# Optimization experiments

Hardware: AMD Instinct MI355X
Metric: run time of the kernel (lower is better)

The kernel has to match this reference:

```python
import jax, jax.numpy as jnp
from jax import lax
import numpy as np
from functools import partial

B, C, H, W = 4, 3, 256, 256
HW = H * W
KCAP = 32          # max tracked components per (batch, class) slot
MAX_ITER = 5
KSIZE = 5


def _depthwise_sum(x, k):
    c = x.shape[1]
    w = jnp.ones((c, 1, k, k), x.dtype)
    return lax.conv_general_dilated(x, w, (1, 1), [(k // 2, k // 2)] * 2,
                                    feature_group_count=c,
                                    dimension_numbers=('NCHW', 'OIHW', 'NCHW'))


def erode(x):
    return (_depthwise_sum(x, KSIZE) >= KSIZE * KSIZE - 0.5).astype(x.dtype)


def dilate(x):
    return (_depthwise_sum(x, KSIZE) > 0.5).astype(x.dtype)


def _maxpool3_int(L):
    return lax.reduce_window(L, jnp.int32(0), lax.max, (1, 1, 3, 3), (1, 1, 1, 1),
                             [(0, 0), (0, 0), (1, 1), (1, 1)])


def label_cc(binary):
    # connected-component labeling by iterated 3x3 max-pool of pixel indices,
    # exactly as find_components_max_pool (labels = max flat pixel index in comp)
    b = lax.stop_gradient(binary) > 0.5
    idx = jnp.arange(HW, dtype=jnp.int32).reshape(1, 1, H, W)
    L0 = jnp.where(b, idx, 0)

    def cond(st):
        return st[1]

    def body(st):
        L, _ = st
        Ln = jnp.where(b, _maxpool3_int(L), 0)
        return Ln, jnp.any(Ln != L)

    L, _ = lax.while_loop(cond, body, (L0, jnp.array(True)))
    return L


def extract_components(Lf, binf):
    # per (b,c): top-KCAP components sorted by comp.sum() = size*label/maxL (desc)
    flat = Lf.reshape(-1)
    sizes = jnp.zeros((HW,), jnp.float32).at[flat].add(binf.reshape(-1))
    idx = jnp.arange(HW, dtype=jnp.int32)
    is_root = (flat == idx) & (flat > 0)  # label 0 excluded, as in torch code
    key = jnp.where(is_root, lax.stop_gradient(sizes) * idx.astype(jnp.float32), -1.0)
    _, top_lab = lax.top_k(key, KCAP)
    valid = key[top_lab] > 0.0
    maxL = jnp.maximum(flat.max(), 1).astype(jnp.float32)
    v = top_lab.astype(jnp.float32)
    s = jnp.where(valid, sizes[top_lab] * v / maxL, 0.0)  # comp.sum()
    lab = jnp.where(valid, top_lab, -1)
    # component tensor = mask * label/maxL, exactly mask*L/max(L) of the original
    comps = (Lf[None] == lab[:, None, None]).astype(jnp.float32) * (v / maxL)[:, None, None]
    return s, comps, valid


def process_step(P, n, bar, s, comps, valid, t):
    # overlaps vs components stored BEFORE this step; new comps within a step
    # are pixel-disjoint so they can never match each other (overlap == 0).
    OV = jnp.einsum('jhw,khw->jk', comps, P)

    def body(carry, inp):
        P, n, bar = carry
        s_j, comp_j, valid_j, ov_j = inp
        best = jnp.argmax(ov_j)
        matched = ov_j[best] > 0.0
        widx = jnp.clip(jnp.where(matched, best, n), 0, KCAP - 1)
        can = valid_j & (matched | (n < KCAP))
        bar = bar.at[widx, t].set(jnp.where(can, s_j, bar[widx, t]))
        add = valid_j & (~matched) & (n < KCAP)
        nw = jnp.minimum(n, KCAP - 1)
        P = P.at[nw].set(jnp.where(add, comp_j, P[nw]))
        return (P, n + add.astype(n.dtype), bar), None

    (P, n, bar), _ = lax.scan(body, (P, n, bar), (s, comps, valid, OV))
    return P, n, bar


def compute_barcodes(binary):
    half = MAX_ITER // 2
    seq = [(binary, half)]
    m = binary
    for t in range(half):
        m = erode(m)
        seq.append((m, half + t + 1))
    m = binary
    for t in range(half):
        m = dilate(m)
        seq.append((m, half - t - 1))
    BC = B * C
    P = jnp.zeros((BC, KCAP, H, W), jnp.float32)
    n = jnp.zeros((BC,), jnp.int32)
    bar = jnp.zeros((BC, KCAP, MAX_ITER), jnp.float32)
    for mp, t in seq:  # fixed 5-step schedule (structural loop)
        L = label_cc(mp).reshape(BC, H, W)
        s, comps, valid = jax.vmap(extract_components)(L, mp.reshape(BC, H, W))
        P, n, bar = jax.vmap(partial(process_step, t=t))(P, n, bar, s, comps, valid)
    return bar.reshape(B, C, KCAP, MAX_ITER), n.reshape(B, C)


def topo_forward(predictions, gumbel, targets):
    y_soft = jax.nn.softmax(predictions + gumbel, axis=1)
    hard = jax.nn.one_hot(jnp.argmax(y_soft, axis=1), C, axis=1, dtype=jnp.float32)
    binary_pred = hard + y_soft - lax.stop_gradient(y_soft)  # straight-through
    binary_tgt = jnp.moveaxis(jax.nn.one_hot(targets, C, dtype=jnp.float32), -1, 1)
    bp, n_p = compute_barcodes(binary_pred)
    bt, n_t = compute_barcodes(binary_tgt)
    k = jnp.arange(KCAP)
    valid_p = k[None, None] < n_p[:, :, None]
    has_t = k[None, None] < n_t[:, :, None]
    pmax = bp.max(-1)
    pmax = jnp.where(pmax > 0, pmax, 1.0)
    tgt = jnp.where(has_t[..., None], bt, 0.0)
    term = jnp.sum((tgt - bp) ** 2, -1) / pmax ** 2
    losses = jnp.sum(jnp.where(valid_p, term, 0.0), axis=(1, 2))
    return losses.mean()  # reduction='mean'


def setup_inputs() -> dict:
    key = jax.random.key(0)
    k1, k2, k3 = jax.random.split(key, 3)
    # blob-like logits: low-res noise upsampled so component counts stay < KCAP
    lo = jax.random.normal(k1, (B, C, 16, 16), jnp.float32)
    predictions = 8.0 * jax.image.resize(lo, (B, C, H, W), 'linear')
    lo_t = jax.random.normal(k2, (B, C, 16, 16), jnp.float32)
    targets = jnp.argmax(jax.image.resize(lo_t, (B, C, H, W), 'linear'), axis=1).astype(jnp.int32)
    u = jax.random.uniform(k3, (B, C, H, W), jnp.float32, minval=1e-6, maxval=1.0 - 1e-6)
    gumbel = -jnp.log(-jnp.log(u))  # standard Gumbel noise (F.gumbel_softmax)
    return {"predictions": predictions, "gumbel": gumbel, "targets": targets}


def reference(predictions, gumbel, targets):
    return topo_forward(predictions, gumbel, targets)
```

## Files before the change

### kernel.cpp

```cpp
#include <hip/hip_runtime.h>

#define NB 4
#define NC 3
#define BC 12
#define HW 65536
#define KCAP 32
#define MAXI 5
#define RUNCAP 16384
#define NSLOT 120
#define NCH 24
#define REGQ 8
#define REGTOT (REGQ*1024)

typedef unsigned long long u64;
typedef unsigned int u32;

__device__ __forceinline__ int uf_find(int* P, int x){
  while (true){
    int p = P[x];
    if (p == x) return x;
    int gp = P[p];
    if (gp == p) return p;
    P[x] = gp;
    x = gp;
  }
}
__device__ __forceinline__ void uf_union_max(int* P, int a, int b){
  while (true){
    a = uf_find(P, a); b = uf_find(P, b);
    if (a == b) return;
    if (a > b){ int t = a; a = b; b = t; }
    int old = atomicCAS(&P[a], a, b);
    if (old == a) return;
    a = old;
  }
}

template<typename F>
__device__ __forceinline__ void walk_runs(const u64* wv, F&& emit){
  int open_s = -1;
  #pragma unroll
  for (int wi = 0; wi < 4; wi++){
    u64 v = wv[wi];
    int base = wi << 6;
    int pos = 0;
    while (pos < 64){
      u64 rem = v >> pos;
      if (open_s >= 0){
        u64 nz = ~rem;
        int z = nz ? __builtin_ctzll(nz) : 64;
        if (z >= 64 - pos){ pos = 64; }
        else { emit(open_s, base + pos + z); open_s = -1; pos += z; }
      } else {
        if (rem == 0ull){ pos = 64; }
        else {
          int o = __builtin_ctzll(rem);
          open_s = base + pos + o;
          pos += o;
        }
      }
    }
  }
  if (open_s >= 0) emit(open_s, 256);
}

__global__ void k_bin(const float* __restrict__ pred, const float* __restrict__ gum,
                      const int* __restrict__ tgt, u64* __restrict__ bmAll){
  int g = blockIdx.x * 256 + threadIdx.x;
  int b = g >> 16, p = g & (HW - 1);
  size_t base = (size_t)b * NC * HW + p;
  float v0 = pred[base]        + gum[base];
  float v1 = pred[base + HW]   + gum[base + HW];
  float v2 = pred[base + 2*HW] + gum[base + 2*HW];
  int a = 0; float m = v0;
  if (v1 > m){ m = v1; a = 1; }
  if (v2 > m){ m = v2; a = 2; }
  int tg = tgt[(size_t)b * HW + p];
  u64 p0 = __ballot(a == 0), p1 = __ballot(a == 1), p2 = __ballot(a == 2);
  u64 t0 = __ballot(tg == 0), t1 = __ballot(tg == 1), t2 = __ballot(tg == 2);
  if ((threadIdx.x & 63) == 0){
    int w = p >> 6;
    int sp = b * NC;
    bmAll[(size_t)(sp + 0) * 1024 + w] = p0;
    bmAll[(size_t)(sp + 1) * 1024 + w] = p1;
    bmAll[(size_t)(sp + 2) * 1024 + w] = p2;
    int st = 60 + b * NC;
    bmAll[(size_t)(st + 0) * 1024 + w] = t0;
    bmAll[(size_t)(st + 1) * 1024 + w] = t1;
    bmAll[(size_t)(st + 2) * 1024 + w] = t2;
  }
}

__global__ void k_morph4(const u64* __restrict__ bmAll, u64* __restrict__ bmAllW,
                         int4 srcs, int4 dsts, int4 flgs){
  int t = blockIdx.x * 256 + threadIdx.x;
  int job = t / 12288, rest = t % 12288;
  int s = rest >> 10, word = rest & 1023;
  int row = word >> 2, w = word & 3;
  int srcG = job == 0 ? srcs.x : job == 1 ? srcs.y : job == 2 ? srcs.z : srcs.w;
  int dstG = job == 0 ? dsts.x : job == 1 ? dsts.y : job == 2 ? dsts.z : dsts.w;
  int er   = job == 0 ? flgs.x : job == 1 ? flgs.y : job == 2 ? flgs.z : flgs.w;
  const u64* bs = bmAll + (size_t)(srcG * BC + s) * 1024;
  u64 res = er ? ~0ull : 0ull;
  for (int dy = -2; dy <= 2; dy++){
    int y = row + dy;
    if (y < 0 || y > 255){ if (er) res = 0; continue; }
    const u64* rw = bs + y * 4;
    u64 m = rw[w];
    u64 l = (w > 0) ? rw[w-1] : 0ull;
    u64 r = (w < 3) ? rw[w+1] : 0ull;
    u64 x1l = (m << 1) | (l >> 63);
    u64 x2l = (m << 2) | (l >> 62);
    u64 x1r = (m >> 1) | (r << 63);
    u64 x2r = (m >> 2) | (r << 62);
    u64 h = er ? (m & x1l & x2l & x1r & x2r) : (m | x1l | x2l | x1r | x2r);
    res = er ? (res & h) : (res | h);
  }
  bmAllW[(size_t)(dstG * BC + s) * 1024 + word] = res;
}

__global__ __launch_bounds__(1024) void k_cc_runs(
    const u64* __restrict__ bmAll, u32* __restrict__ rootPk ,
    int* __restrict__ selCnt, float* __restrict__ sSel, float* __restrict__ scaleSel){
  __shared__ int par[RUNCAP];
  __shared__ u32 pkz[RUNCAP];
  __shared__ int rs[257];
  __shared__ u32 used[RUNCAP/32];
  __shared__ int selRoot[KCAP];
  __shared__ u64 wred[16];
  __shared__ u64 bestS;
  __shared__ int nRootS, lmS, nSelS;
  int u = blockIdx.x, t = threadIdx.x;
  bool rowT = t < 256;
  u64 wv[4] = {0,0,0,0};
  int nr = 0;
  if (rowT){
    const u64* bp = bmAll + (size_t)u * 1024 + t * 4;
    #pragma unroll
    for (int i = 0; i < 4; i++) wv[i] = bp[i];
    walk_runs(wv, [&](int a, int b){ (void)a; (void)b; nr++; });
    rs[t] = nr;
  }
  if (t == 0){ nRootS = 0; lmS = 0; nSelS = 0; }
  if (t < KCAP) selRoot[t] = -1;
  for (int i = t; i < RUNCAP/32; i += 1024) used[i] = 0;
  __syncthreads();
  for (int d = 1; d < 256; d <<= 1){
    int add = 0;
    if (rowT && t >= d) add = rs[t - d];
    __syncthreads();
    if (rowT) rs[t] += add;
    __syncthreads();
  }
  int incl = rowT ? rs[t] : 0;
  __syncthreads();
  if (rowT) rs[t] = incl - nr;
  if (t == 255) rs[256] = incl;
  __syncthreads();
  int NR = rs[256];
  int NRc = NR < RUNCAP ? NR : RUNCAP;
  int myBase = rowT ? rs[t] : 0;
  size_t base = (size_t)u * RUNCAP;
  for (int i = t; i < NRc; i += 1024) par[i] = i;
  if (rowT){
    int o = myBase;
    walk_runs(wv, [&](int a, int b){
      if (o < RUNCAP) pkz[o] = ((u32)t << 16) | ((u32)a << 8) | (u32)(b - 1);
      o++;
    });
  }
  __syncthreads();
  for (int i = t; i < NRc; i += 1024){
    u32 v = pkz[i];
    int r = v >> 16;
    if (r == 0) continue;
    int s2 = (int)((v >> 8) & 255), E2 = (int)(v & 255);
    int a0 = rs[r-1], a1 = rs[r];
    if (a1 > NRc) a1 = NRc;
    if (a0 >= a1) continue;
    int lo = a0, hi = a1;
    while (lo < hi){
      int mid = (lo + hi) >> 1;
      if ((int)(pkz[mid] & 255) >= s2 - 1) hi = mid; else lo = mid + 1;
    }
    for (int j = lo; j < a1; j++){
      int s1 = (int)((pkz[j] >> 8) & 255);
      if (s1 > E2 + 1) break;
      uf_union_max(par, i, j);
    }
  }
  __syncthreads();
  for (int i = t; i < NRc; i += 1024){
    int r = i, p = par[r];
    while (p != r){ r = p; p = par[r]; }
    par[i] = r;
  }
  __syncthreads();
  {
    int lm = 0;
    for (int i = t; i < NRc; i += 1024){
      u32 v = pkz[i];
      int s0 = (int)((v >> 8) & 255), E = (int)(v & 255);
      int root = par[i] & 16383;
      atomicAdd(&par[root], (E - s0 + 1) << 14);
      int pix = (int)(v >> 16) * 256 + E;
      lm = max(lm, pix);
      if (root == i && pix > 0){
        int pos = atomicAdd(&nRootS, 1);
        rootPk[base + pos] = ((u32)pix << 14) | (u32)i;
      }
    }
    atomicMax(&lmS, lm);
  }
  __syncthreads();
  float maxLf = (float)(lmS >= 1 ? lmS : 1);
  int nRoots = nRootS;
  u64 myKeys[REGQ];
  #pragma unroll
  for (int q = 0; q < REGQ; q++){
    myKeys[q] = 0;
    int e = q * 1024 + t;
    if (e < nRoots){
      u32 v = rootPk[base + e];
      int lab = (int)(v >> 14);
      int idx = (int)(v & 16383);
      float key = (float)(((u32)par[idx]) >> 14) * (float)lab;
      myKeys[q] = ((u64)__float_as_uint(key) << 32) | ((u64)(0xFFFFu - (u32)lab) << 16)
                | ((u64)q << 10) | (u64)t;
    }
  }
  for (int r = 0; r < KCAP; r++){
    u64 b = 0;
    #pragma unroll
    for (int q = 0; q < REGQ; q++) b = (myKeys[q] > b) ? myKeys[q] : b;
    if (nRoots > REGTOT){
      for (int e = REGTOT + t; e < nRoots; e += 1024){
        if ((used[e >> 5] >> (e & 31)) & 1u) continue;
        u32 v = rootPk[base + e];
        int lab = (int)(v >> 14);
        int idx = (int)(v & 16383);
        float key = (float)(((u32)par[idx]) >> 14) * (float)lab;
        u64 cand = ((u64)__float_as_uint(key) << 32) | ((u64)(0xFFFFu - (u32)lab) << 16)
                 | 0x8000u | (u64)e;
        b = (cand > b) ? cand : b;
      }
    }
    #pragma unroll
    for (int off = 32; off > 0; off >>= 1){
      u64 o = __shfl_xor(b, off);
      b = (o > b) ? o : b;
    }
    if ((t & 63) == 0) wred[t >> 6] = b;
    __syncthreads();
    if (t == 0){
      u64 m = 0;
      #pragma unroll
      for (int wq = 0; wq < 16; wq++) m = (wred[wq] > m) ? wred[wq] : m;
      bestS = m;
    }
    __syncthreads();
    u64 bestAll = bestS;
    if (bestAll == 0){
      if (t == 0){
        for (int q = r; q < KCAP; q++){ sSel[u*KCAP + q] = 0.0f; scaleSel[u*KCAP + q] = 0.0f; }
      }
      break;
    }
    if (!(bestAll & 0x8000ull)){
      #pragma unroll
      for (int q = 0; q < REGQ; q++) if (myKeys[q] == bestAll) myKeys[q] = 0;
    }
    if (t == 0){
      int e;
      if (bestAll & 0x8000ull){
        e = (int)(bestAll & 0x3FFF);
        used[e >> 5] |= 1u << (e & 31);
      } else {
        e = (int)((bestAll >> 10) & 7) * 1024 + (int)(bestAll & 1023);
      }
      int lab = 0xFFFF - (int)((bestAll >> 16) & 0xFFFF);
      selRoot[r] = (int)(rootPk[base + e] & 16383);
      sSel[u*KCAP + r]     = __uint_as_float((u32)(bestAll >> 32)) / maxLf;
      scaleSel[u*KCAP + r] = (float)lab / maxLf;
    }
    __syncthreads();
  }
  __syncthreads();
  for (int i = t; i < NRc; i += 1024) pkz[i] = 255u;
  __syncthreads();
  if (t < KCAP && selRoot[t] >= 0) pkz[selRoot[t]] = (u32)t;
  __syncthreads();
  if (rowT){
    int o = myBase;
    walk_runs(wv, [&](int a, int b){
      if (o < RUNCAP){
        u32 j = pkz[par[o] & 16383];
        if (j < KCAP){
          int pos = atomicAdd(&nSelS, 1);
          rootPk[base + pos] = (j << 24) | ((u32)t << 16) | ((u32)a << 8) | (u32)(b - 1);
        }
      }
      o++;
    });
  }
  __syncthreads();
  if (t == 0) selCnt[u] = nSelS;
}

__global__ __launch_bounds__(1024) void k_chainall(
    const u32* __restrict__ selRuns, const int* __restrict__ selCnt,
    const float* __restrict__ sSel, const float* __restrict__ scaleSel,
    float* __restrict__ barP, float* __restrict__ barT,
    int* __restrict__ n24, u64* __restrict__ Pbm){
  int w = blockIdx.x, t = threadIdx.x;
  int pass = w / 12, s = w % 12;
  __shared__ int cnt[KCAP*KCAP];
  __shared__ float spL[KCAP];
  __shared__ int add_dst[KCAP];
  __shared__ int bestA[KCAP];
  __shared__ float bvA[KCAP];
  __shared__ int nS;
  if (t < KCAP) spL[t] = 0.0f;
  if (t == 0) nS = 0;
  float* bar = (pass ? barT : barP) + (size_t)s * KCAP * MAXI;
  u64* Pb = Pbm + (size_t)w * KCAP * 1024;
  #pragma unroll 1
  for (int st = 0; st < 5; st++){
    int u = (pass * 5 + st) * BC + s;
    int tval = (st < 3) ? st + 2 : (st == 3 ? 1 : 0);
    for (int i = t; i < KCAP*KCAP; i += 1024) cnt[i] = 0;
    __syncthreads();
    int n0 = nS;
    int NS = selCnt[u];
    const u32* rp = selRuns + (size_t)u * RUNCAP;
    for (int i = t; i < NS; i += 1024){
      u32 v = rp[i];
      int j = v >> 24;
      int row = (v >> 16) & 255, s0 = (v >> 8) & 255, E = (int)(v & 255);
      int w0 = s0 >> 6, w1 = E >> 6;
      int acc[KCAP];
      #pragma unroll
      for (int k2 = 0; k2 < KCAP; k2++) acc[k2] = 0;
      for (int wi = w0; wi <= w1; wi++){
        int lo = max(s0, wi << 6), hi = min(E + 1, (wi << 6) + 64);
        u64 mask = (hi - lo == 64) ? ~0ull : ((((u64)1 << (hi - lo)) - 1) << (lo - (wi << 6)));
        int wofs = row * 4 + wi;
        #pragma unroll
        for (int k2 = 0; k2 < KCAP; k2++){
          if (k2 < n0) acc[k2] += __popcll(Pb[(size_t)k2 * 1024 + wofs] & mask);
        }
      }
      #pragma unroll
      for (int k2 = 0; k2 < KCAP; k2++){
        if (k2 < n0 && acc[k2]) atomicAdd(&cnt[j*KCAP + k2], acc[k2]);
      }
    }
    __syncthreads();
    if (t < KCAP){
      float sn = scaleSel[(size_t)u*KCAP + t];
      int best = 0; float bv = 0.0f;
      if (sn > 0.0f && n0 > 0){
        bv = sn * spL[0] * (float)cnt[t*KCAP + 0];
        for (int k2 = 1; k2 < n0; k2++){
          float ov = sn * spL[k2] * (float)cnt[t*KCAP + k2];
          if (ov > bv){ bv = ov; best = k2; }
        }
      }
      bestA[t] = best; bvA[t] = bv;
    }
    __syncthreads();
    if (t == 0){
      int n = n0;
      for (int j = 0; j < KCAP; j++){
        add_dst[j] = -1;
        float sv = scaleSel[(size_t)u*KCAP + j];
        if (sv <= 0.0f) continue;
        if (bvA[j] > 0.0f){
          bar[bestA[j]*MAXI + tval] = sSel[(size_t)u*KCAP + j];
        } else if (n < KCAP){
          bar[n*MAXI + tval] = sSel[(size_t)u*KCAP + j];
          spL[n] = sv;
          add_dst[j] = n;
          n++;
        }
      }
      nS = n;
    }
    __syncthreads();
    for (int j = 0; j < KCAP; j++){
      int d = add_dst[j];
      if (d < 0) continue;
      u64* dst = Pb + (size_t)d * 1024;
      for (int x = t; x < 1024; x += 1024) dst[x] = 0ull;
    }
    __syncthreads();
    for (int i = t; i < NS; i += 1024){
      u32 v = rp[i];
      int j = v >> 24;
      int d = add_dst[j];
      if (d < 0) continue;
      int row = (v >> 16) & 255, s0 = (v >> 8) & 255, E = (int)(v & 255);
      int w0 = s0 >> 6, w1 = E >> 6;
      u64* dst = Pb + (size_t)d * 1024 + row * 4;
      for (int wi = w0; wi <= w1; wi++){
        int lo = max(s0, wi << 6), hi = min(E + 1, (wi << 6) + 64);
        u64 mask = (hi - lo == 64) ? ~0ull : ((((u64)1 << (hi - lo)) - 1) << (lo - (wi << 6)));
        atomicOr(&dst[wi], mask);
      }
    }
    __syncthreads();
  }
  if (t == 0) n24[w] = nS;
}

__global__ void k_loss(const float* __restrict__ barP, const float* __restrict__ barT,
                       const int* __restrict__ n24, float* __restrict__ out){
  __shared__ float red[512];
  int t = threadIdx.x;
  float val = 0.0f;
  if (t < BC * KCAP){
    int s = t >> 5, k = t & 31;
    int np = n24[s], nt = n24[12 + s];
    if (k < np){
      const float* bp = barP + (size_t)(s*KCAP + k)*MAXI;
      float pmax = bp[0];
      #pragma unroll
      for (int q = 1; q < MAXI; q++) pmax = fmaxf(pmax, bp[q]);
      if (!(pmax > 0.0f)) pmax = 1.0f;
      float acc = 0.0f;
      #pragma unroll
      for (int q = 0; q < MAXI; q++){
        float tv = (k < nt) ? barT[(size_t)(s*KCAP + k)*MAXI + q] : 0.0f;
        float d = tv - bp[q];
        acc += d * d;
      }
      val = acc / (pmax * pmax);
    }
  }
  red[t] = val;
  __syncthreads();
  for (int off = 256; off > 0; off >>= 1){
    if (t < off) red[t] += red[t + off];
    __syncthreads();
  }
  if (t == 0) out[0] = red[0] * 0.25f;
}

extern "C" void kernel_launch(void* const* d_in, const int* in_sizes, int n_in,
                              void* d_out, int out_size, void* d_ws, size_t ws_size,
                              hipStream_t stream){
  const float* pred = (const float*)d_in[0];
  const float* gum  = (const float*)d_in[1];
  const int*   tgt  = (const int*)d_in[2];
  float* out = (float*)d_out;
  char* ws = (char*)d_ws;
  size_t off = 0;
  auto alloc = [&](size_t bytes)->char*{
    char* p = ws + off;
    off += (bytes + 255) & ~(size_t)255;
    return p;
  };
  u64* bmAll   = (u64*)alloc((size_t)NSLOT*1024*8);
  u32* rootPk  = (u32*)alloc((size_t)NSLOT*RUNCAP*4);
  int* selCnt  = (int*)alloc(NSLOT*4);
  float* sSel     = (float*)alloc((size_t)NSLOT*KCAP*4);
  float* scaleSel = (float*)alloc((size_t)NSLOT*KCAP*4);
  u64* Pbm     = (u64*)alloc((size_t)NCH*KCAP*1024*8);
  int* n24     = (int*)alloc(NCH*4);
  size_t zbytes = (size_t)(BC*KCAP*MAXI*2)*4;
  char* zreg = alloc(zbytes);
  float* barP = (float*)zreg;
  float* barT = barP + BC*KCAP*MAXI;
  if (off > ws_size) return;

  hipMemsetAsync(zreg, 0, zbytes, stream);
  k_bin<<<(NB*HW)/256,256,0,stream>>>(pred, gum, tgt, bmAll);
  k_morph4<<<192,256,0,stream>>>(bmAll, bmAll, make_int4(0,0,5,5), make_int4(1,3,6,8), make_int4(1,0,1,0));
  k_morph4<<<192,256,0,stream>>>(bmAll, bmAll, make_int4(1,3,6,8), make_int4(2,4,7,9), make_int4(1,0,1,0));
  k_cc_runs<<<NSLOT,1024,0,stream>>>(bmAll, rootPk, selCnt, sSel, scaleSel);
  k_chainall<<<NCH,1024,0,stream>>>(rootPk, selCnt, sSel, scaleSel, barP, barT, n24, Pbm);
  k_loss<<<1,512,0,stream>>>(barP, barT, n24, out);
}
```

Before: 260.8 us.

## Restructure top-K selection in CC kernel to per-wave candidates and shuffle scans

Replaces the shared-memory Hillis-Steele prefix scan with wave-level shuffle scans. Top-KCAP selection no longer does a block-wide reduction with two barriers per round: each wave extracts its own top-32 candidates with no block barriers, then one wave merges them. Root keys are now built directly from the par/pkz arrays, which drops the atomic root list in global memory, and selected runs are written deterministically through a second scan instead of atomics. Each thread now holds 16 register keys, raising register pressure in a 1024-thread block.

```diff
diff --git a/kernel.cpp b/kernel.cpp
--- a/kernel.cpp
+++ b/kernel.cpp
@@ -9,8 +9,7 @@
 #define RUNCAP 16384
 #define NSLOT 120
 #define NCH 24
-#define REGQ 8
-#define REGTOT (REGQ*1024)
+#define REGQ 16
 
 typedef unsigned long long u64;
 typedef unsigned int u32;
@@ -120,17 +119,18 @@
 }
 
 __global__ __launch_bounds__(1024) void k_cc_runs(
-    const u64* __restrict__ bmAll, u32* __restrict__ rootPk ,
+    const u64* __restrict__ bmAll, u32* __restrict__ selRuns,
     int* __restrict__ selCnt, float* __restrict__ sSel, float* __restrict__ scaleSel){
   __shared__ int par[RUNCAP];
   __shared__ u32 pkz[RUNCAP];
   __shared__ int rs[257];
-  __shared__ u32 used[RUNCAP/32];
+  __shared__ u64 wcand[16*KCAP];
+  __shared__ u64 selKeys[KCAP];
   __shared__ int selRoot[KCAP];
-  __shared__ u64 wred[16];
-  __shared__ u64 bestS;
-  __shared__ int nRootS, lmS, nSelS;
+  __shared__ int wsum[4], wsum2[4];
+  __shared__ int lmS;
   int u = blockIdx.x, t = threadIdx.x;
+  int lane = t & 63, wid = t >> 6;
   bool rowT = t < 256;
   u64 wv[4] = {0,0,0,0};
   int nr = 0;
@@ -139,28 +139,28 @@
     #pragma unroll
     for (int i = 0; i < 4; i++) wv[i] = bp[i];
     walk_runs(wv, [&](int a, int b){ (void)a; (void)b; nr++; });
-    rs[t] = nr;
-  }
-  if (t == 0){ nRootS = 0; lmS = 0; nSelS = 0; }
-  if (t < KCAP) selRoot[t] = -1;
-  for (int i = t; i < RUNCAP/32; i += 1024) used[i] = 0;
-  __syncthreads();
-  for (int d = 1; d < 256; d <<= 1){
-    int add = 0;
-    if (rowT && t >= d) add = rs[t - d];
-    __syncthreads();
-    if (rowT) rs[t] += add;
-    __syncthreads();
-  }
-  int incl = rowT ? rs[t] : 0;
-  __syncthreads();
-  if (rowT) rs[t] = incl - nr;
-  if (t == 255) rs[256] = incl;
-  __syncthreads();
+  }
+  if (t == 0) lmS = 0;
+  {
+    int v = nr;
+    #pragma unroll
+    for (int d = 1; d < 64; d <<= 1){
+      int o = __shfl_up(v, d);
+      if (lane >= d) v += o;
+    }
+    if (rowT && lane == 63) wsum[wid] = v;
+    __syncthreads();
+    if (rowT){
+      int pre = 0;
+      for (int q = 0; q < wid; q++) pre += wsum[q];
+      rs[t] = pre + v - nr;
+      if (t == 255) rs[256] = pre + v;
+    }
+    __syncthreads();
+  }
   int NR = rs[256];
   int NRc = NR < RUNCAP ? NR : RUNCAP;
   int myBase = rowT ? rs[t] : 0;
-  size_t base = (size_t)u * RUNCAP;
   for (int i = t; i < NRc; i += 1024) par[i] = i;
   if (rowT){
     int o = myBase;
@@ -201,110 +201,124 @@
     for (int i = t; i < NRc; i += 1024){
       u32 v = pkz[i];
       int s0 = (int)((v >> 8) & 255), E = (int)(v & 255);
-      int root = par[i] & 16383;
-      atomicAdd(&par[root], (E - s0 + 1) << 14);
-      int pix = (int)(v >> 16) * 256 + E;
-      lm = max(lm, pix);
-      if (root == i && pix > 0){
-        int pos = atomicAdd(&nRootS, 1);
-        rootPk[base + pos] = ((u32)pix << 14) | (u32)i;
-      }
-    }
-    atomicMax(&lmS, lm);
+      atomicAdd(&par[par[i] & 16383], (E - s0 + 1) << 14);
+      lm = max(lm, (int)(v >> 16) * 256 + E);
+    }
+    #pragma unroll
+    for (int off = 32; off > 0; off >>= 1) lm = max(lm, __shfl_xor(lm, off));
+    if (lane == 0) atomicMax(&lmS, lm);
   }
   __syncthreads();
   float maxLf = (float)(lmS >= 1 ? lmS : 1);
-  int nRoots = nRootS;
   u64 myKeys[REGQ];
   #pragma unroll
   for (int q = 0; q < REGQ; q++){
     myKeys[q] = 0;
-    int e = q * 1024 + t;
-    if (e < nRoots){
-      u32 v = rootPk[base + e];
-      int lab = (int)(v >> 14);
-      int idx = (int)(v & 16383);
-      float key = (float)(((u32)par[idx]) >> 14) * (float)lab;
-      myKeys[q] = ((u64)__float_as_uint(key) << 32) | ((u64)(0xFFFFu - (u32)lab) << 16)
-                | ((u64)q << 10) | (u64)t;
-    }
-  }
+    int i = q * 1024 + t;
+    if (i < NRc){
+      int pv = par[i];
+      if ((pv & 16383) == i){
+        u32 v = pkz[i];
+        int lab = (int)(v >> 16) * 256 + (int)(v & 255);
+        if (lab > 0){
+          float key = (float)((u32)pv >> 14) * (float)lab;
+          myKeys[q] = ((u64)__float_as_uint(key) << 32) | ((u64)(0xFFFFu - (u32)lab) << 16)
+                    | (u64)i;
+        }
+      }
+    }
+  }
+  if (lane < KCAP) wcand[wid*KCAP + lane] = 0;
   for (int r = 0; r < KCAP; r++){
     u64 b = 0;
     #pragma unroll
     for (int q = 0; q < REGQ; q++) b = (myKeys[q] > b) ? myKeys[q] : b;
-    if (nRoots > REGTOT){
-      for (int e = REGTOT + t; e < nRoots; e += 1024){
-        if ((used[e >> 5] >> (e & 31)) & 1u) continue;
-        u32 v = rootPk[base + e];
-        int lab = (int)(v >> 14);
-        int idx = (int)(v & 16383);
-        float key = (float)(((u32)par[idx]) >> 14) * (float)lab;
-        u64 cand = ((u64)__float_as_uint(key) << 32) | ((u64)(0xFFFFu - (u32)lab) << 16)
-                 | 0x8000u | (u64)e;
-        b = (cand > b) ? cand : b;
-      }
-    }
     #pragma unroll
     for (int off = 32; off > 0; off >>= 1){
       u64 o = __shfl_xor(b, off);
       b = (o > b) ? o : b;
     }
-    if ((t & 63) == 0) wred[t >> 6] = b;
-    __syncthreads();
-    if (t == 0){
-      u64 m = 0;
-      #pragma unroll
-      for (int wq = 0; wq < 16; wq++) m = (wred[wq] > m) ? wred[wq] : m;
-      bestS = m;
-    }
-    __syncthreads();
-    u64 bestAll = bestS;
-    if (bestAll == 0){
-      if (t == 0){
-        for (int q = r; q < KCAP; q++){ sSel[u*KCAP + q] = 0.0f; scaleSel[u*KCAP + q] = 0.0f; }
-      }
-      break;
-    }
-    if (!(bestAll & 0x8000ull)){
-      #pragma unroll
-      for (int q = 0; q < REGQ; q++) if (myKeys[q] == bestAll) myKeys[q] = 0;
-    }
-    if (t == 0){
-      int e;
-      if (bestAll & 0x8000ull){
-        e = (int)(bestAll & 0x3FFF);
-        used[e >> 5] |= 1u << (e & 31);
-      } else {
-        e = (int)((bestAll >> 10) & 7) * 1024 + (int)(bestAll & 1023);
-      }
-      int lab = 0xFFFF - (int)((bestAll >> 16) & 0xFFFF);
-      selRoot[r] = (int)(rootPk[base + e] & 16383);
-      sSel[u*KCAP + r]     = __uint_as_float((u32)(bestAll >> 32)) / maxLf;
-      scaleSel[u*KCAP + r] = (float)lab / maxLf;
-    }
-    __syncthreads();
+    if (b == 0) break;
+    #pragma unroll
+    for (int q = 0; q < REGQ; q++) if (myKeys[q] == b) myKeys[q] = 0;
+    if (lane == 0) wcand[wid*KCAP + r] = b;
+  }
+  __syncthreads();
+  if (wid == 0){
+    u64 c[8];
+    #pragma unroll
+    for (int q = 0; q < 8; q++) c[q] = wcand[q*64 + lane];
+    if (lane < KCAP) selKeys[lane] = 0;
+    for (int r = 0; r < KCAP; r++){
+      u64 b = 0;
+      #pragma unroll
+      for (int q = 0; q < 8; q++) b = (c[q] > b) ? c[q] : b;
+      #pragma unroll
+      for (int off = 32; off > 0; off >>= 1){
+        u64 o = __shfl_xor(b, off);
+        b = (o > b) ? o : b;
+      }
+      if (b == 0) break;
+      #pragma unroll
+      for (int q = 0; q < 8; q++) if (c[q] == b) c[q] = 0;
+      if (lane == 0) selKeys[r] = b;
+    }
+  }
+  __syncthreads();
+  if (t < KCAP){
+    u64 k = selKeys[t];
+    if (k){
+      int lab = 0xFFFF - (int)((k >> 16) & 0xFFFF);
+      selRoot[t] = (int)(k & 0x3FFF);
+      sSel[u*KCAP + t]     = __uint_as_float((u32)(k >> 32)) / maxLf;
+      scaleSel[u*KCAP + t] = (float)lab / maxLf;
+    } else {
+      selRoot[t] = -1;
+      sSel[u*KCAP + t] = 0.0f;
+      scaleSel[u*KCAP + t] = 0.0f;
+    }
   }
   __syncthreads();
   for (int i = t; i < NRc; i += 1024) pkz[i] = 255u;
   __syncthreads();
   if (t < KCAP && selRoot[t] >= 0) pkz[selRoot[t]] = (u32)t;
   __syncthreads();
+  int c = 0;
   if (rowT){
     int o = myBase;
     walk_runs(wv, [&](int a, int b){
-      if (o < RUNCAP){
-        u32 j = pkz[par[o] & 16383];
-        if (j < KCAP){
-          int pos = atomicAdd(&nSelS, 1);
-          rootPk[base + pos] = (j << 24) | ((u32)t << 16) | ((u32)a << 8) | (u32)(b - 1);
-        }
-      }
+      if (o < RUNCAP && pkz[par[o] & 16383] < KCAP) c++;
       o++;
     });
   }
-  __syncthreads();
-  if (t == 0) selCnt[u] = nSelS;
+  {
+    int v = c;
+    #pragma unroll
+    for (int d = 1; d < 64; d <<= 1){
+      int o = __shfl_up(v, d);
+      if (lane >= d) v += o;
+    }
+    if (rowT && lane == 63) wsum2[wid] = v;
+    __syncthreads();
+    if (rowT){
+      int pre = 0;
+      for (int q = 0; q < wid; q++) pre += wsum2[q];
+      int w = pre + v - c;
+      size_t base = (size_t)u * RUNCAP;
+      int o = myBase;
+      walk_runs(wv, [&](int a, int b){
+        if (o < RUNCAP){
+          u32 j = pkz[par[o] & 16383];
+          if (j < KCAP){
+            selRuns[base + w] = (j << 24) | ((u32)t << 16) | ((u32)a << 8) | (u32)(b - 1);
+            w++;
+          }
+        }
+        o++;
+      });
+    }
+    if (t == 0) selCnt[u] = wsum2[0] + wsum2[1] + wsum2[2] + wsum2[3];
+  }
 }
 
 __global__ __launch_bounds__(1024) void k_chainall(
@@ -461,7 +475,7 @@
     return p;
   };
   u64* bmAll   = (u64*)alloc((size_t)NSLOT*1024*8);
-  u32* rootPk  = (u32*)alloc((size_t)NSLOT*RUNCAP*4);
+  u32* selRuns = (u32*)alloc((size_t)NSLOT*RUNCAP*4);
   int* selCnt  = (int*)alloc(NSLOT*4);
   float* sSel     = (float*)alloc((size_t)NSLOT*KCAP*4);
   float* scaleSel = (float*)alloc((size_t)NSLOT*KCAP*4);
@@ -477,7 +491,7 @@
   k_bin<<<(NB*HW)/256,256,0,stream>>>(pred, gum, tgt, bmAll);
   k_morph4<<<192,256,0,stream>>>(bmAll, bmAll, make_int4(0,0,5,5), make_int4(1,3,6,8), make_int4(1,0,1,0));
   k_morph4<<<192,256,0,stream>>>(bmAll, bmAll, make_int4(1,3,6,8), make_int4(2,4,7,9), make_int4(1,0,1,0));
-  k_cc_runs<<<NSLOT,1024,0,stream>>>(bmAll, rootPk, selCnt, sSel, scaleSel);
-  k_chainall<<<NCH,1024,0,stream>>>(rootPk, selCnt, sSel, scaleSel, barP, barT, n24, Pbm);
+  k_cc_runs<<<NSLOT,1024,0,stream>>>(bmAll, selRuns, selCnt, sSel, scaleSel);
+  k_chainall<<<NCH,1024,0,stream>>>(selRuns, selCnt, sSel, scaleSel, barP, barT, n24, Pbm);
   k_loss<<<1,512,0,stream>>>(barP, barT, n24, out);
 }
```

Measured after the change: 411.6 us. +57.9%, slower.
